# Optimization experiments

Measured on AMD Instinct MI355X. Metric: run time of the kernel, lower is better.

Reference implementation:

```python
import jax, jax.numpy as jnp
import numpy as np

N, C, H, W = 8, 32, 16, 16   # input batch / channels / spatial
OC = 64                       # out_channels
K = 3                         # kernel_size
PAD = 1                       # padding (stride=1, dilation=1 -> output HxW == input HxW)
WIDTH = 8                     # hwcfg['width']
RLEN = 2 ** WIDTH             # Sobol RNG sequence length = 256
CKK = C * K * K               # unfolded patch length = 288
B = N * H * W                 # flattened patch batch = 2048


def _sobol_rng():
    # 1-D Sobol sequence == van der Corput base-2: bit-reversed counter scaled to [0, 2^width)
    idx = np.arange(RLEN, dtype=np.uint32)
    rev = np.zeros(RLEN, dtype=np.uint32)
    for b in range(WIDTH):
        rev |= ((idx >> b) & 1) << (WIDTH - 1 - b)
    return jnp.asarray(rev.astype(np.float32))


def setup_inputs() -> dict:
    key = jax.random.key(0)
    k1, k2, k3, k4, k5, k6 = jax.random.split(key, 6)
    # unary (stochastic bitstream) input: bits in {0,1}
    x = jax.random.bernoulli(k1, 0.5, (N, C, H, W)).astype(jnp.float32)
    # BinGen, bipolar: binary = round((v + 1)/2 * 2^width), v in [-1, 1]
    w = jax.random.uniform(k2, (OC, CKK), minval=-1.0, maxval=1.0)
    w_bin = jnp.round((w + 1.0) / 2.0 * RLEN)
    b = jax.random.uniform(k3, (OC,), minval=-1.0, maxval=1.0)
    b_bin = jnp.round((b + 1.0) / 2.0 * RLEN)
    rng = _sobol_rng()
    # mid-stream BSGen index state (per patch position, as the module cats to batch copies)
    wrdx_i1 = jax.random.randint(k4, (B, OC, CKK), 0, RLEN, dtype=jnp.int32)
    wrdx_i0 = jax.random.randint(k5, (B, OC, CKK), 0, RLEN, dtype=jnp.int32)
    brdx = jax.random.randint(k6, (OC,), 0, RLEN, dtype=jnp.int32)
    return {"x": x, "w_bin": w_bin, "b_bin": b_bin, "rng": rng,
            "wrdx_i1": wrdx_i1, "wrdx_i0": wrdx_i0, "brdx": brdx}


def _unfold(x):
    # even cycle -> ConstantPad2d(pad, 0); torch.nn.functional.unfold ordering (c, kh, kw)
    xp = jnp.pad(x, ((0, 0), (0, 0), (PAD, PAD), (PAD, PAD)))
    cols = jnp.stack([xp[:, :, i:i + H, j:j + W] for i in range(K) for j in range(K)], axis=2)
    # [N, C, K*K, H, W] -> [N, CKK, L] -> [N, L, CKK] -> [B, CKK]
    return cols.reshape(N, CKK, H * W).transpose(0, 2, 1).reshape(B, CKK)


def reference(x, w_bin, b_bin, rng, wrdx_i1, wrdx_i0, brdx):
    ib1 = _unfold(x)                                                        # [B, CKK], bits
    # BSGen: bit = (binary_value > rng[index % RLEN])
    wbit1 = (w_bin[None] > rng[wrdx_i1 % RLEN]).astype(jnp.float32)         # [B, OC, CKK]
    wbit0 = 1.0 - (w_bin[None] > rng[wrdx_i0 % RLEN]).astype(jnp.float32)   # [B, OC, CKK]
    # bipolar parallel counter: x*w1 path + (1-x)*(1-w) path
    obin = (jnp.einsum('bk,bok->bo', ib1, wbit1)
            + jnp.einsum('bk,bok->bo', 1.0 - ib1, wbit0))                   # [B, OC]
    bbit = (b_bin > rng[brdx % RLEN]).astype(jnp.float32)                   # [OC]
    # fold(1,1): [N, L, OC] -> [N, OC, H, W]
    out = obin.reshape(N, H * W, OC).transpose(0, 2, 1).reshape(N, OC, H, W)
    return out + bbit[None, :, None, None]
```

## Files before the change

### kernel.cpp

```cpp
#include <hip/hip_runtime.h>


#define CH   32
#define HH   16
#define WW   16
#define OCN  64
#define CKK  288
#define LL   256
#define BB   2048

__device__ __forceinline__ float sobol_val(int idx) {
    return (float)(__brev((unsigned)idx) >> 24);
}

__device__ __forceinline__ float contrib(float xb, float wv, int i1, int i0) {
    float t1  = (wv > sobol_val(i1)) ? 1.f : 0.f;
    float nt0 = (wv > sobol_val(i0)) ? 0.f : 1.f;
    return (xb != 0.f) ? t1 : nt0;
}

__global__ __launch_bounds__(256) void fsuconv_kernel(
    const float* __restrict__ x,
    const float* __restrict__ w_bin,
    const float* __restrict__ b_bin,
    const int*   __restrict__ wrdx1,
    const int*   __restrict__ wrdx0,
    const int*   __restrict__ brdx,
    float*       __restrict__ out)
{
    __shared__ __align__(16) float ib1[CKK];

    const int blk = blockIdx.x;
    const int b   = blk >> 4;
    const int og  = blk & 15;
    const int n   = b >> 8;
    const int l   = b & 255;
    const int h   = l >> 4;
    const int w0  = l & 15;

    for (int k = threadIdx.x; k < CKK; k += 256) {
        int c  = k / 9;
        int r  = k - c * 9;
        int kh = r / 3;
        int kw = r - kh * 3;
        int ih = h + kh - 1;
        int iw = w0 + kw - 1;
        float v = 0.f;
        if ((unsigned)ih < 16u && (unsigned)iw < 16u)
            v = x[((n * CH + c) * HH + ih) * WW + iw];
        ib1[k] = v;
    }
    __syncthreads();

    const int wave = threadIdx.x >> 6;
    const int lane = threadIdx.x & 63;
    const int o    = og * 4 + wave;

    const size_t rowoff = ((size_t)b * OCN + o) * CKK;
    const int4*   r1 = (const int4*)(wrdx1 + rowoff);
    const int4*   r0 = (const int4*)(wrdx0 + rowoff);
    const float4* wr = (const float4*)(w_bin + (size_t)o * CKK);

    float sum = 0.f;

    {
        int4   a  = r1[lane];
        int4   c0 = r0[lane];
        float4 wv = wr[lane];
        float4 xv = *(const float4*)&ib1[lane * 4];
        sum += contrib(xv.x, wv.x, a.x, c0.x);
        sum += contrib(xv.y, wv.y, a.y, c0.y);
        sum += contrib(xv.z, wv.z, a.z, c0.z);
        sum += contrib(xv.w, wv.w, a.w, c0.w);
    }
    if (lane < 8) {
        int4   a  = r1[64 + lane];
        int4   c0 = r0[64 + lane];
        float4 wv = wr[64 + lane];
        float4 xv = *(const float4*)&ib1[256 + lane * 4];
        sum += contrib(xv.x, wv.x, a.x, c0.x);
        sum += contrib(xv.y, wv.y, a.y, c0.y);
        sum += contrib(xv.z, wv.z, a.z, c0.z);
        sum += contrib(xv.w, wv.w, a.w, c0.w);
    }

    for (int off = 32; off > 0; off >>= 1)
        sum += __shfl_down(sum, off);

    if (lane == 0) {
        float bb = (b_bin[o] > sobol_val(brdx[o])) ? 1.f : 0.f;
        out[((size_t)n * OCN + o) * LL + l] = sum + bb;
    }
}

extern "C" void kernel_launch(void* const* d_in, const int* in_sizes, int n_in,
                              void* d_out, int out_size, void* d_ws, size_t ws_size,
                              hipStream_t stream) {
    const float* x     = (const float*)d_in[0];
    const float* w_bin = (const float*)d_in[1];
    const float* b_bin = (const float*)d_in[2];
    const int*   wrdx1 = (const int*)d_in[4];
    const int*   wrdx0 = (const int*)d_in[5];
    const int*   brdx  = (const int*)d_in[6];
    float*       out   = (float*)d_out;

    dim3 grid(BB * 16);
    dim3 block(256);
    fsuconv_kernel<<<grid, block, 0, stream>>>(x, w_bin, b_bin, wrdx1, wrdx0, brdx, out);
}
```

Measured before the change: 315.7 us.

## Process 16 output channels per wave with ballot-popcount counting and double-buffered loads

The grid shrinks to one block per patch, with each wave looping over 16 output channels. Loads alternate between two register buffers so the next row is in flight while the current one is computed. The per-element float compares and the shuffle reduction are replaced by integer key compares of bit-reversed indices, wave ballots combined with input-bit masks, and popcount. This cuts block launch count, repeated input unfolding, and the reduction cost. In exchange each block does more serial work and occupancy may drop from higher register use and fewer blocks.

```diff
diff --git a/kernel.cpp b/kernel.cpp
--- a/kernel.cpp
+++ b/kernel.cpp
@@ -13,13 +13,19 @@
     return (float)(__brev((unsigned)idx) >> 24);
 }
 
-__device__ __forceinline__ float contrib(float xb, float wv, int i1, int i0) {
-    float t1  = (wv > sobol_val(i1)) ? 1.f : 0.f;
-    float nt0 = (wv > sobol_val(i0)) ? 0.f : 1.f;
-    return (xb != 0.f) ? t1 : nt0;
+__device__ __forceinline__ unsigned wkey(float wv) {
+    unsigned wi = (unsigned)wv;
+    return (wi >= 256u) ? 0xFFFFFFFFu : (wi << 24);
 }
 
-__global__ __launch_bounds__(256) void fsuconv_kernel(
+struct RowBuf {
+    int4   a, c;
+    float4 wv;
+    int4   at, ct;
+    float4 wt;
+};
+
+__global__ __launch_bounds__(256, 4) void fsuconv_kernel(
     const float* __restrict__ x,
     const float* __restrict__ w_bin,
     const float* __restrict__ b_bin,
@@ -29,14 +35,13 @@
     float*       __restrict__ out)
 {
     __shared__ __align__(16) float ib1[CKK];
+    __shared__ float bbit[OCN];
 
-    const int blk = blockIdx.x;
-    const int b   = blk >> 4;
-    const int og  = blk & 15;
-    const int n   = b >> 8;
-    const int l   = b & 255;
-    const int h   = l >> 4;
-    const int w0  = l & 15;
+    const int b  = blockIdx.x;
+    const int n  = b >> 8;
+    const int l  = b & 255;
+    const int h  = l >> 4;
+    const int w0 = l & 15;
 
     for (int k = threadIdx.x; k < CKK; k += 256) {
         int c  = k / 9;
@@ -50,46 +55,80 @@
             v = x[((n * CH + c) * HH + ih) * WW + iw];
         ib1[k] = v;
     }
+    if (threadIdx.x < OCN) {
+        int o = threadIdx.x;
+        bbit[o] = (b_bin[o] > sobol_val(brdx[o])) ? 1.f : 0.f;
+    }
     __syncthreads();
 
     const int wave = threadIdx.x >> 6;
     const int lane = threadIdx.x & 63;
-    const int o    = og * 4 + wave;
 
-    const size_t rowoff = ((size_t)b * OCN + o) * CKK;
-    const int4*   r1 = (const int4*)(wrdx1 + rowoff);
-    const int4*   r0 = (const int4*)(wrdx0 + rowoff);
-    const float4* wr = (const float4*)(w_bin + (size_t)o * CKK);
+    float4 xv  = ((const float4*)ib1)[lane];
+    float4 xtv = make_float4(0.f, 0.f, 0.f, 0.f);
+    if (lane < 8) xtv = ((const float4*)ib1)[64 + lane];
 
-    float sum = 0.f;
+    const unsigned long long xm0 = __ballot(xv.x != 0.f);
+    const unsigned long long xm1 = __ballot(xv.y != 0.f);
+    const unsigned long long xm2 = __ballot(xv.z != 0.f);
+    const unsigned long long xm3 = __ballot(xv.w != 0.f);
+    const unsigned long long xt0 = __ballot(xtv.x != 0.f);
+    const unsigned long long xt1 = __ballot(xtv.y != 0.f);
+    const unsigned long long xt2 = __ballot(xtv.z != 0.f);
+    const unsigned long long xt3 = __ballot(xtv.w != 0.f);
 
-    {
-        int4   a  = r1[lane];
-        int4   c0 = r0[lane];
-        float4 wv = wr[lane];
-        float4 xv = *(const float4*)&ib1[lane * 4];
-        sum += contrib(xv.x, wv.x, a.x, c0.x);
-        sum += contrib(xv.y, wv.y, a.y, c0.y);
-        sum += contrib(xv.z, wv.z, a.z, c0.z);
-        sum += contrib(xv.w, wv.w, a.w, c0.w);
-    }
-    if (lane < 8) {
-        int4   a  = r1[64 + lane];
-        int4   c0 = r0[64 + lane];
-        float4 wv = wr[64 + lane];
-        float4 xv = *(const float4*)&ib1[256 + lane * 4];
-        sum += contrib(xv.x, wv.x, a.x, c0.x);
-        sum += contrib(xv.y, wv.y, a.y, c0.y);
-        sum += contrib(xv.z, wv.z, a.z, c0.z);
-        sum += contrib(xv.w, wv.w, a.w, c0.w);
-    }
+    const int obase = wave * 16;
+    const int*   p1 = wrdx1 + ((size_t)b * OCN + obase) * CKK;
+    const int*   p0 = wrdx0 + ((size_t)b * OCN + obase) * CKK;
+    const float* pw = w_bin + (size_t)obase * CKK;
 
-    for (int off = 32; off > 0; off >>= 1)
-        sum += __shfl_down(sum, off);
+    RowBuf A = {}, B = {};
 
-    if (lane == 0) {
-        float bb = (b_bin[o] > sobol_val(brdx[o])) ? 1.f : 0.f;
-        out[((size_t)n * OCN + o) * LL + l] = sum + bb;
+    auto loadrow = [&](RowBuf& rb, int j) {
+        const int4*   q1 = (const int4*)(p1 + j * CKK);
+        const int4*   q0 = (const int4*)(p0 + j * CKK);
+        const float4* qw = (const float4*)(pw + j * CKK);
+        rb.a  = q1[lane];
+        rb.c  = q0[lane];
+        rb.wv = qw[lane];
+        if (lane < 8) {
+            rb.at = q1[64 + lane];
+            rb.ct = q0[64 + lane];
+            rb.wt = qw[64 + lane];
+        }
+    };
+
+    auto chunk = [&](float wf, int a1, int a0,
+                     unsigned long long xm) -> unsigned long long {
+        unsigned k = wkey(wf);
+        unsigned long long m1 = __ballot(k > __brev((unsigned)a1));
+        unsigned long long m0 = __ballot(k > __brev((unsigned)a0));
+        return (xm & m1) | (~xm & ~m0);
+    };
+
+    auto computerow = [&](const RowBuf& rb, int j) {
+        unsigned cnt = 0;
+        cnt += __popcll(chunk(rb.wv.x, rb.a.x, rb.c.x, xm0));
+        cnt += __popcll(chunk(rb.wv.y, rb.a.y, rb.c.y, xm1));
+        cnt += __popcll(chunk(rb.wv.z, rb.a.z, rb.c.z, xm2));
+        cnt += __popcll(chunk(rb.wv.w, rb.a.w, rb.c.w, xm3));
+        cnt += __popcll(chunk(rb.wt.x, rb.at.x, rb.ct.x, xt0) & 0xFFull);
+        cnt += __popcll(chunk(rb.wt.y, rb.at.y, rb.ct.y, xt1) & 0xFFull);
+        cnt += __popcll(chunk(rb.wt.z, rb.at.z, rb.ct.z, xt2) & 0xFFull);
+        cnt += __popcll(chunk(rb.wt.w, rb.at.w, rb.ct.w, xt3) & 0xFFull);
+        if (lane == 0) {
+            int o = obase + j;
+            out[((size_t)n * OCN + o) * LL + l] = (float)cnt + bbit[o];
+        }
+    };
+
+    loadrow(A, 0);
+    #pragma unroll
+    for (int j = 0; j < 16; j += 2) {
+        loadrow(B, j + 1);
+        computerow(A, j);
+        if (j + 2 < 16) loadrow(A, j + 2);
+        computerow(B, j + 1);
     }
 }
 
@@ -104,7 +143,7 @@
     const int*   brdx  = (const int*)d_in[6];
     float*       out   = (float*)d_out;
 
-    dim3 grid(BB * 16);
+    dim3 grid(BB);
     dim3 block(256);
     fsuconv_kernel<<<grid, block, 0, stream>>>(x, w_bin, b_bin, wrdx1, wrdx0, brdx, out);
 }
```

New measurement: 322.1 us. +2.0%, slower.

## Split into prepass and bit-packed ballot/popcount streaming kernel with pipelined row loads

Applied to the files above, without the earlier changes.

A prepass kernel packs the unfolded input bits into 64-bit ballot masks per patch, converts weights to shifted integer thresholds, and precomputes the bias bits. The main kernel then compares weights against bit-reversed indices, combines the results with ballots and bitwise masks, and counts with popcount, which removes the float compares and the shuffle reduction. Each wave now handles four output channels, with manual double-buffered row loads separated by sched_barriers. The cost is a second launch and some workspace traffic, while the main cost, streaming the large index arrays, stays the same.

```diff
diff --git a/kernel.cpp b/kernel.cpp
--- a/kernel.cpp
+++ b/kernel.cpp
@@ -9,88 +9,136 @@
 #define LL   256
 #define BB   2048
 
-__device__ __forceinline__ float sobol_val(int idx) {
-    return (float)(__brev((unsigned)idx) >> 24);
+#define WS_XM_OFF 0
+#define WS_WK_OFF 131072
+#define WS_BB_OFF 204800
+
+__device__ __forceinline__ float unf_val(const float* __restrict__ x,
+                                         int n, int h, int w0, int k) {
+    int c  = k / 9;
+    int r  = k - c * 9;
+    int kh = r / 3;
+    int kw = r - kh * 3;
+    int ih = h + kh - 1;
+    int iw = w0 + kw - 1;
+    float v = 0.f;
+    if ((unsigned)ih < 16u && (unsigned)iw < 16u)
+        v = x[((n * CH + c) * HH + ih) * WW + iw];
+    return v;
 }
 
-__device__ __forceinline__ float contrib(float xb, float wv, int i1, int i0) {
-    float t1  = (wv > sobol_val(i1)) ? 1.f : 0.f;
-    float nt0 = (wv > sobol_val(i0)) ? 0.f : 1.f;
-    return (xb != 0.f) ? t1 : nt0;
+__global__ __launch_bounds__(256) void fsu_pre(
+    const float* __restrict__ x, const float* __restrict__ w_bin,
+    const float* __restrict__ b_bin, const int* __restrict__ brdx,
+    unsigned long long* __restrict__ xm, unsigned* __restrict__ wk,
+    float* __restrict__ bb)
+{
+    if (blockIdx.x == 512) {
+        for (int i = threadIdx.x; i < OCN * CKK; i += 256) {
+            unsigned wi = (unsigned)w_bin[i];
+            wk[i] = (wi >= 256u) ? 0xFFFFFFFFu : (wi << 24);
+        }
+        if (threadIdx.x < OCN) {
+            int o = threadIdx.x;
+            float rv = (float)(__brev((unsigned)brdx[o]) >> 24);
+            bb[o] = (b_bin[o] > rv) ? 1.f : 0.f;
+        }
+        return;
+    }
+    const int wave = threadIdx.x >> 6;
+    const int lane = threadIdx.x & 63;
+    const int b = blockIdx.x * 4 + wave;
+    const int n = b >> 8, l = b & 255;
+    const int h = l >> 4, w0 = l & 15;
+
+    unsigned long long m[8];
+    #pragma unroll
+    for (int e = 0; e < 4; ++e)
+        m[e] = __ballot(unf_val(x, n, h, w0, lane * 4 + e) != 0.f);
+    #pragma unroll
+    for (int e = 0; e < 4; ++e)
+        m[4 + e] = __ballot(unf_val(x, n, h, w0, 256 + (lane & 7) * 4 + e) != 0.f);
+
+    if (lane == 0) {
+        #pragma unroll
+        for (int e = 0; e < 8; ++e) xm[(size_t)b * 8 + e] = m[e];
+    }
 }
 
-__global__ __launch_bounds__(256) void fsuconv_kernel(
-    const float* __restrict__ x,
-    const float* __restrict__ w_bin,
-    const float* __restrict__ b_bin,
-    const int*   __restrict__ wrdx1,
-    const int*   __restrict__ wrdx0,
-    const int*   __restrict__ brdx,
-    float*       __restrict__ out)
+struct Row {
+    int4  a, c;
+    uint4 k;
+    int4  at, ct;
+    uint4 kt;
+};
+
+__device__ __forceinline__ void load_row(Row& r, const int* __restrict__ p1,
+                                         const int* __restrict__ p0,
+                                         const unsigned* __restrict__ pw,
+                                         int j, int lane, int tl) {
+    const int4*  q1 = (const int4*)(p1 + j * CKK);
+    const int4*  q0 = (const int4*)(p0 + j * CKK);
+    const uint4* qw = (const uint4*)(pw + j * CKK);
+    r.a  = q1[lane]; r.c  = q0[lane]; r.k  = qw[lane];
+    r.at = q1[tl];   r.ct = q0[tl];   r.kt = qw[tl];
+}
+
+__device__ __forceinline__ unsigned long long chunkm(unsigned k, int a1, int a0,
+                                                     unsigned long long xm) {
+    unsigned long long m1 = __ballot(k > __brev((unsigned)a1));
+    unsigned long long m0 = __ballot(k > __brev((unsigned)a0));
+    return (xm & m1) | (~xm & ~m0);
+}
+
+__global__ __launch_bounds__(256) void fsu_stream(
+    const int* __restrict__ wrdx1, const int* __restrict__ wrdx0,
+    const unsigned* __restrict__ wk, const unsigned long long* __restrict__ xm,
+    const float* __restrict__ bb, float* __restrict__ out)
 {
-    __shared__ __align__(16) float ib1[CKK];
-
-    const int blk = blockIdx.x;
-    const int b   = blk >> 4;
-    const int og  = blk & 15;
-    const int n   = b >> 8;
-    const int l   = b & 255;
-    const int h   = l >> 4;
-    const int w0  = l & 15;
-
-    for (int k = threadIdx.x; k < CKK; k += 256) {
-        int c  = k / 9;
-        int r  = k - c * 9;
-        int kh = r / 3;
-        int kw = r - kh * 3;
-        int ih = h + kh - 1;
-        int iw = w0 + kw - 1;
-        float v = 0.f;
-        if ((unsigned)ih < 16u && (unsigned)iw < 16u)
-            v = x[((n * CH + c) * HH + ih) * WW + iw];
-        ib1[k] = v;
-    }
-    __syncthreads();
-
+    const int blk  = blockIdx.x;
+    const int b    = blk >> 2;
+    const int og   = blk & 3;
     const int wave = threadIdx.x >> 6;
     const int lane = threadIdx.x & 63;
-    const int o    = og * 4 + wave;
+    const int obase = og * 16 + wave * 4;
+    const int n = b >> 8, l = b & 255;
+    const int tl = 64 + (lane & 7);
 
-    const size_t rowoff = ((size_t)b * OCN + o) * CKK;
-    const int4*   r1 = (const int4*)(wrdx1 + rowoff);
-    const int4*   r0 = (const int4*)(wrdx0 + rowoff);
-    const float4* wr = (const float4*)(w_bin + (size_t)o * CKK);
+    const unsigned long long* xb = xm + (size_t)b * 8;
+    const unsigned long long xm0 = xb[0], xm1 = xb[1], xm2 = xb[2], xm3 = xb[3];
+    const unsigned long long xt0 = xb[4], xt1 = xb[5], xt2 = xb[6], xt3 = xb[7];
 
-    float sum = 0.f;
+    const int* p1 = wrdx1 + ((size_t)b * OCN + obase) * CKK;
+    const int* p0 = wrdx0 + ((size_t)b * OCN + obase) * CKK;
+    const unsigned* pw = wk + (size_t)obase * CKK;
+    float* po = out + ((size_t)n * OCN + obase) * LL + l;
 
-    {
-        int4   a  = r1[lane];
-        int4   c0 = r0[lane];
-        float4 wv = wr[lane];
-        float4 xv = *(const float4*)&ib1[lane * 4];
-        sum += contrib(xv.x, wv.x, a.x, c0.x);
-        sum += contrib(xv.y, wv.y, a.y, c0.y);
-        sum += contrib(xv.z, wv.z, a.z, c0.z);
-        sum += contrib(xv.w, wv.w, a.w, c0.w);
-    }
-    if (lane < 8) {
-        int4   a  = r1[64 + lane];
-        int4   c0 = r0[64 + lane];
-        float4 wv = wr[64 + lane];
-        float4 xv = *(const float4*)&ib1[256 + lane * 4];
-        sum += contrib(xv.x, wv.x, a.x, c0.x);
-        sum += contrib(xv.y, wv.y, a.y, c0.y);
-        sum += contrib(xv.z, wv.z, a.z, c0.z);
-        sum += contrib(xv.w, wv.w, a.w, c0.w);
-    }
+    auto docompute = [&](const Row& r, int j) {
+        unsigned cnt = 0;
+        cnt += __popcll(chunkm(r.k.x,  r.a.x,  r.c.x,  xm0));
+        cnt += __popcll(chunkm(r.k.y,  r.a.y,  r.c.y,  xm1));
+        cnt += __popcll(chunkm(r.k.z,  r.a.z,  r.c.z,  xm2));
+        cnt += __popcll(chunkm(r.k.w,  r.a.w,  r.c.w,  xm3));
+        cnt += __popcll(chunkm(r.kt.x, r.at.x, r.ct.x, xt0) & 0xFFull);
+        cnt += __popcll(chunkm(r.kt.y, r.at.y, r.ct.y, xt1) & 0xFFull);
+        cnt += __popcll(chunkm(r.kt.z, r.at.z, r.ct.z, xt2) & 0xFFull);
+        cnt += __popcll(chunkm(r.kt.w, r.at.w, r.ct.w, xt3) & 0xFFull);
+        if (lane == 0)
+            po[j * LL] = (float)cnt + bb[obase + j];
+    };
 
-    for (int off = 32; off > 0; off >>= 1)
-        sum += __shfl_down(sum, off);
-
-    if (lane == 0) {
-        float bb = (b_bin[o] > sobol_val(brdx[o])) ? 1.f : 0.f;
-        out[((size_t)n * OCN + o) * LL + l] = sum + bb;
-    }
+    Row A, B;
+    load_row(A, p1, p0, pw, 0, lane, tl);
+    load_row(B, p1, p0, pw, 1, lane, tl);
+    __builtin_amdgcn_sched_barrier(0);
+    docompute(A, 0);
+    load_row(A, p1, p0, pw, 2, lane, tl);
+    __builtin_amdgcn_sched_barrier(0);
+    docompute(B, 1);
+    load_row(B, p1, p0, pw, 3, lane, tl);
+    __builtin_amdgcn_sched_barrier(0);
+    docompute(A, 2);
+    docompute(B, 3);
 }
 
 extern "C" void kernel_launch(void* const* d_in, const int* in_sizes, int n_in,
@@ -104,7 +152,10 @@
     const int*   brdx  = (const int*)d_in[6];
     float*       out   = (float*)d_out;
 
-    dim3 grid(BB * 16);
-    dim3 block(256);
-    fsuconv_kernel<<<grid, block, 0, stream>>>(x, w_bin, b_bin, wrdx1, wrdx0, brdx, out);
+    unsigned long long* xm = (unsigned long long*)((char*)d_ws + WS_XM_OFF);
+    unsigned*           wk = (unsigned*)((char*)d_ws + WS_WK_OFF);
+    float*              bb = (float*)((char*)d_ws + WS_BB_OFF);
+
+    fsu_pre<<<dim3(513), dim3(256), 0, stream>>>(x, w_bin, b_bin, brdx, xm, wk, bb);
+    fsu_stream<<<dim3(BB * 4), dim3(256), 0, stream>>>(wrdx1, wrdx0, wk, xm, bb, out);
 }
```

After: 330.2 us. 1.05x slower.
